# Optimization experiments

Measured on AMD Instinct MI355X. Metric: run time of the kernel, lower is better.

The kernel has to match this reference:

```python
import jax, jax.numpy as jnp
import numpy as np

C_, A_, B_ = 1, 128, 128          # image_size
H, Z, T, N = 512, 128, 16, 32     # h_dim, z_dim, steps, attention grid
EPS = 1e-8
BATCH = 256
PATCH = C_ * N * N                # read/write patch size (C_=1)
IN_ENC = 2 * PATCH + H


def gru_cell(x, h, W_ih, W_hh, b_ih, b_hh):
    gi = x @ W_ih.T + b_ih
    gh = h @ W_hh.T + b_hh
    i_r, i_z, i_n = jnp.split(gi, 3, axis=-1)
    h_r, h_z, h_n = jnp.split(gh, 3, axis=-1)
    r = jax.nn.sigmoid(i_r + h_r)
    z = jax.nn.sigmoid(i_z + h_z)
    n = jnp.tanh(i_n + r * h_n)
    return (1.0 - z) * n + z * h


def filterbank(gt, delta, two_sigma_sq, num_pixels):
    # gt, delta: [b,1]; two_sigma_sq: [b,1,1]
    g = 0.5 * (num_pixels + 1) * (gt + 1.0)                       # [b,1]
    grid = jnp.arange(N, dtype=jnp.float32) - 0.5 * (N - 1)       # [N]
    mu = g + grid[None, :] * delta                                # [b,N]
    pix = jnp.arange(num_pixels, dtype=jnp.float32)               # [P]
    F = jnp.exp(-(pix[None, None, :] - mu[:, :, None]) ** 2 / two_sigma_sq)
    return F / jnp.maximum(F.sum(axis=-1, keepdims=True), EPS)    # [b,N,P]


def get_filterbanks(h_dec, W_attn, b_attn):
    p = h_dec @ W_attn.T + b_attn                                 # [b,5]
    gt_x, gt_y, log_ss, log_dt, log_g = [p[:, i:i + 1] for i in range(5)]
    two_sigma_sq = (2.0 * jnp.exp(log_ss))[:, :, None]            # [b,1,1]
    delta = (max(A_, B_) - 1) * jnp.exp(log_dt) / (N - 1)         # [b,1]
    gamma = jnp.exp(log_g)                                        # [b,1]
    F_x = filterbank(gt_x, delta, two_sigma_sq, A_)               # [b,N,A]
    F_y = filterbank(gt_y, delta, two_sigma_sq, B_)               # [b,N,B]
    return F_x, F_y, gamma


def draw_forward(x, eps, W_ih_enc, W_hh_enc, b_ih_enc, b_hh_enc,
                 W_ih_dec, W_hh_dec, b_ih_dec, b_hh_dec,
                 W_mu, b_mu, W_ls, b_ls, W_wr, b_wr,
                 W_ra, b_ra, W_wa, b_wa):
    b = x.shape[0]
    xf = x.reshape(b, -1)                                         # [b, A*B]
    reconsts0 = jnp.zeros_like(xf)
    h0 = jnp.zeros((b, H), dtype=xf.dtype)

    def step(carry, eps_t):
        reconsts, h_enc, h_dec = carry
        # NOTE: faithful to original: reconsts[-1] is last batch row, broadcast
        x_hat = xf - jax.nn.sigmoid(reconsts[-1])
        # ---- read with attention ----
        F_x, F_y, gamma = get_filterbanks(h_dec, W_ra, b_ra)
        F_x_t = jnp.swapaxes(F_x, -1, -2)                         # [b,A,N]
        img = xf.reshape(b, A_, B_)
        img_hat = x_hat.reshape(b, A_, B_)
        x_attn = (F_y @ img @ F_x_t).reshape(b, -1)               # [b,N*N]
        xh_attn = (F_y @ img_hat @ F_x_t).reshape(b, -1)
        r = gamma * jnp.concatenate([x_attn, xh_attn], axis=1)    # [b,2*N*N]
        # ---- encoder GRU ----
        h_enc = gru_cell(jnp.concatenate([r, h_dec], axis=1), h_enc,
                         W_ih_enc, W_hh_enc, b_ih_enc, b_hh_enc)
        # ---- sample z ~ Q ----
        mu = h_enc @ W_mu.T + b_mu
        sigma = jnp.exp(h_enc @ W_ls.T + b_ls)
        z = mu + eps_t * sigma
        # ---- decoder GRU ----
        h_dec = gru_cell(z, h_dec, W_ih_dec, W_hh_dec, b_ih_dec, b_hh_dec)
        # ---- write with attention ----
        F_xw, F_yw, gamma_w = get_filterbanks(h_dec, W_wa, b_wa)
        w = (h_dec @ W_wr.T + b_wr).reshape(b, N, N)
        wr = (jnp.swapaxes(F_yw, -1, -2) @ w @ F_xw).reshape(b, -1) / gamma_w
        return (reconsts + wr, h_enc, h_dec), None

    (reconsts, _, _), _ = jax.lax.scan(step, (reconsts0, h0, h0), eps)
    return jax.nn.sigmoid(reconsts).reshape(-1, C_, A_, B_)


def setup_inputs() -> dict:
    key = jax.random.key(0)
    ks = jax.random.split(key, 24)
    s = 0.02
    inp = {
        "x": jax.random.uniform(ks[0], (BATCH, C_, A_, B_), jnp.float32),
        "eps": jax.random.normal(ks[1], (T, BATCH, Z), jnp.float32),
        "W_ih_enc": jax.random.normal(ks[2], (3 * H, IN_ENC), jnp.float32) * s,
        "W_hh_enc": jax.random.normal(ks[3], (3 * H, H), jnp.float32) * s,
        "b_ih_enc": jnp.zeros((3 * H,), jnp.float32),
        "b_hh_enc": jnp.zeros((3 * H,), jnp.float32),
        "W_ih_dec": jax.random.normal(ks[4], (3 * H, Z), jnp.float32) * s,
        "W_hh_dec": jax.random.normal(ks[5], (3 * H, H), jnp.float32) * s,
        "b_ih_dec": jnp.zeros((3 * H,), jnp.float32),
        "b_hh_dec": jnp.zeros((3 * H,), jnp.float32),
        "W_mu": jax.random.normal(ks[6], (Z, H), jnp.float32) * s,
        "b_mu": jnp.zeros((Z,), jnp.float32),
        "W_ls": jax.random.normal(ks[7], (Z, H), jnp.float32) * s,
        "b_ls": jnp.zeros((Z,), jnp.float32),
        "W_wr": jax.random.normal(ks[8], (PATCH, H), jnp.float32) * s,
        "b_wr": jnp.zeros((PATCH,), jnp.float32),
        "W_ra": jax.random.normal(ks[9], (5, H), jnp.float32) * s,
        "b_ra": jnp.zeros((5,), jnp.float32),
        "W_wa": jax.random.normal(ks[10], (5, H), jnp.float32) * s,
        "b_wa": jnp.zeros((5,), jnp.float32),
    }
    return inp


def reference(x, eps, W_ih_enc, W_hh_enc, b_ih_enc, b_hh_enc,
              W_ih_dec, W_hh_dec, b_ih_dec, b_hh_dec,
              W_mu, b_mu, W_ls, b_ls, W_wr, b_wr,
              W_ra, b_ra, W_wa, b_wa):
    return draw_forward(x, eps, W_ih_enc, W_hh_enc, b_ih_enc, b_hh_enc,
                        W_ih_dec, W_hh_dec, b_ih_dec, b_hh_dec,
                        W_mu, b_mu, W_ls, b_ls, W_wr, b_wr,
                        W_ra, b_ra, W_wa, b_wa)
```

## Files before the change

kernel.cpp:

```cpp
#include <hip/hip_runtime.h>
#include <math.h>

#define BATCHN 256
#define HDIM 512
#define ZDIM 128
#define NGRID 32
#define ABDIM 128
#define IMGSZ 16384
#define ENCIN 2560
#define G3 1536
#define SLAB (BATCHN*G3)

typedef __attribute__((ext_vector_type(8))) short short8;
typedef __attribute__((ext_vector_type(4))) float f32x4;

__device__ __forceinline__ float sigmoidf_(float x){ return 1.0f/(1.0f+expf(-x)); }

__device__ __forceinline__ ushort f2bf_rne(float f){
    union{float f; uint u;} x; x.f=f;
    uint r = (x.u + 0x7FFFu + ((x.u>>16)&1u)) >> 16;
    return (ushort)r;
}
__device__ __forceinline__ float bf2f(ushort h){
    union{uint u; float f;} y; y.u = ((uint)h)<<16;
    return y.f;
}

__global__ void init_slast_k(float* __restrict__ s_last){
    int i = blockIdx.x*256 + threadIdx.x;
    s_last[i] = 0.5f;
}

__global__ void conv_wh_k(const float* __restrict__ W, ushort* __restrict__ Wh, int n4){
    int i = blockIdx.x*256 + threadIdx.x;
    if(i>=n4) return;
    float4 v = ((const float4*)W)[i];
    ushort4 hv;
    hv.x=f2bf_rne(v.x); hv.y=f2bf_rne(v.y); hv.z=f2bf_rne(v.z); hv.w=f2bf_rne(v.w);
    ((ushort4*)Wh)[i] = hv;
}

__device__ __forceinline__ void stage_swz(const ushort* __restrict__ g, int K,
        int grow0, int kb, ushort* lds, int tid){
    int wv = tid>>6, lane = tid&63;
    #pragma unroll
    for(int q=0;q<2;q++){
        int instr = wv*2 + q;
        int rl = instr*8 + (lane>>3);
        int sc = (lane&7) ^ (lane>>3);
        const ushort* src = g + (size_t)(grow0+rl)*K + kb + sc*8;
        ushort* dst = lds + instr*512;
        __builtin_amdgcn_global_load_lds((const __attribute__((address_space(1))) void*)src,
                                         (__attribute__((address_space(3))) void*)dst, 16, 0, 0);
    }
}

__device__ __forceinline__ short8 lds_read_swz(const ushort* arr, int r, int slot){
    return *(const short8*)&arr[r*64 + ((slot ^ (r&7))<<3)];
}

__device__ __forceinline__ short8 lds_read_swz128(const ushort* arr, int r, int slot16){
    return lds_read_swz(arr + (slot16>>3)*4096, r, slot16&7);
}

__device__ __forceinline__ void attn_params_dev512(const float* __restrict__ h,
        const float* __restrict__ W, const float* __restrict__ bvec,
        float* red5, float* pp, int tid){
    float accp[5];
    #pragma unroll
    for(int i=0;i<5;i++) accp[i]=0.f;
    for(int k=tid;k<HDIM;k+=512){
        float hv = h[k];
        #pragma unroll
        for(int i=0;i<5;i++) accp[i] += hv*W[i*HDIM+k];
    }
    int wv = tid>>6;
    #pragma unroll
    for(int i=0;i<5;i++){
        float a = accp[i];
        #pragma unroll
        for(int o=32;o>0;o>>=1) a += __shfl_down(a,o);
        if((tid&63)==0) red5[i*8+wv]=a;
    }
    __syncthreads();
    if(tid<5){
        float s = bvec[tid];
        #pragma unroll
        for(int w2=0;w2<8;w2++) s += red5[tid*8+w2];
        pp[tid]=s;
    }
    __syncthreads();
}

__device__ __forceinline__ void fill_fb_T(float* fxT, float* fyT, const float* pp, int tid){
    float gx = 64.5f*(pp[0]+1.0f);
    float gy = 64.5f*(pp[1]+1.0f);
    float tss = 2.0f*expf(pp[2]);
    float delta = (127.0f/31.0f)*expf(pp[3]);
    int rr = tid>>3;
    int q  = tid&7;
    int j  = rr&31;
    bool isY = rr>=32;
    float mu = (isY?gy:gx) + ((float)j-15.5f)*delta;
    float v[16]; float s=0.f;
    #pragma unroll
    for(int i=0;i<16;i++){
        float d = (float)(q*16+i)-mu;
        float e = expf(-d*d/tss);
        v[i]=e; s+=e;
    }
    s += __shfl_xor(s,1); s += __shfl_xor(s,2); s += __shfl_xor(s,4);
    float inv = 1.0f/fmaxf(s,1e-8f);
    float* dst = isY? fyT : fxT;
    #pragma unroll
    for(int i=0;i<16;i++) dst[(q*16+i)*32 + j] = v[i]*inv;
    __syncthreads();
}

__device__ __forceinline__ void fill_fb_R(float (*fx)[ABDIM+1], float (*fy)[ABDIM+1], const float* pp, int tid){
    float gx = 64.5f*(pp[0]+1.0f);
    float gy = 64.5f*(pp[1]+1.0f);
    float tss = 2.0f*expf(pp[2]);
    float delta = (127.0f/31.0f)*expf(pp[3]);
    int rr = tid>>3;
    int q  = tid&7;
    int j  = rr&31;
    bool isY = rr>=32;
    float mu = (isY?gy:gx) + ((float)j-15.5f)*delta;
    float v[16]; float s=0.f;
    #pragma unroll
    for(int i=0;i<16;i++){
        float d = (float)(q*16+i)-mu;
        float e = expf(-d*d/tss);
        v[i]=e; s+=e;
    }
    s += __shfl_xor(s,1); s += __shfl_xor(s,2); s += __shfl_xor(s,4);
    float inv = 1.0f/fmaxf(s,1e-8f);
    float* rowp = isY? &fy[j][0] : &fx[j][0];
    #pragma unroll
    for(int i=0;i<16;i++) rowp[q*16+i] = v[i]*inv;
    __syncthreads();
}

__global__ __launch_bounds__(512) void read_attn_k(const float* __restrict__ xf, const float* __restrict__ s_last,
        const float* __restrict__ hdec, const ushort* __restrict__ Hd_h, const ushort* __restrict__ Hd_l,
        const float* __restrict__ W_ra, const float* __restrict__ b_ra,
        ushort* __restrict__ Eh, ushort* __restrict__ El){
    __shared__ float smem[4096 + 8256 + 48];
    float* sFxT = smem;
    float* sFyT = smem + 4096;
    float* tmp  = smem + 4096;
    float* red5 = smem + 4096 + 8256;
    float* pp   = red5 + 40;
    int bb = blockIdx.x >> 1, half = blockIdx.x & 1;
    int tid = threadIdx.x;
    const float* h = hdec + bb*HDIM;
    attn_params_dev512(h, W_ra, b_ra, red5, pp, tid);
    float gamma = expf(pp[4]);
    fill_fb_T(sFxT, sFyT, pp, tid);

    const float* img = xf + (size_t)bb*IMGSZ;
    int c = tid & 127;
    int jg = tid >> 7;
    int jbase = half*16 + jg*4;
    float acc0[4], accS[4];
    #pragma unroll
    for(int i=0;i<4;i++){ acc0[i]=0.f; accS[i]=0.f; }
    for(int k=0;k<ABDIM;k++){
        float s  = img[k*ABDIM + c];
        float sl = s_last[k*ABDIM + c];
        float4 f0 = *(const float4*)&sFyT[k*32 + jbase];
        acc0[0]+=f0.x*s;  acc0[1]+=f0.y*s;  acc0[2]+=f0.z*s;  acc0[3]+=f0.w*s;
        accS[0]+=f0.x*sl; accS[1]+=f0.y*sl; accS[2]+=f0.z*sl; accS[3]+=f0.w*sl;
    }
    __syncthreads();
    #pragma unroll
    for(int i=0;i<4;i++){
        int jl = jg*4+i;
        tmp[0*16*129 + jl*129 + c] = acc0[i];
        tmp[1*16*129 + jl*129 + c] = acc0[i] - accS[i];
    }
    __syncthreads();
    {
        int i2 = tid & 15;
        int jl = (tid>>4) & 15;
        int p  = tid >> 8;
        float a0=0.f, a1=0.f;
        for(int cc=0; cc<ABDIM; cc++){
            float tv = tmp[p*16*129 + jl*129 + cc];
            a0 += tv*sFxT[cc*32 + i2*2];
            a1 += tv*sFxT[cc*32 + i2*2 + 1];
        }
        float o0 = gamma*a0, o1 = gamma*a1;
        int j = half*16 + jl;
        ushort h0=f2bf_rne(o0), h1=f2bf_rne(o1);
        ushort2 oh; oh.x=h0; oh.y=h1;
        ushort2 ol; ol.x=f2bf_rne(o0-bf2f(h0)); ol.y=f2bf_rne(o1-bf2f(h1));
        size_t off = (size_t)bb*ENCIN + p*1024 + j*NGRID + i2*2;
        *(ushort2*)(Eh + off) = oh;
        *(ushort2*)(El + off) = ol;
    }
    if(half==0){
        int i = tid;
        Eh[(size_t)bb*ENCIN + 2048 + i] = Hd_h[(size_t)bb*HDIM + i];
        El[(size_t)bb*ENCIN + 2048 + i] = Hd_l[(size_t)bb*HDIM + i];
    }
}

__device__ void gemm_one(const ushort* __restrict__ Agh, const ushort* __restrict__ Agl,
        const ushort* __restrict__ Wh,
        int K, int k0, int kiters, int row0, int col0, int Nn, float* __restrict__ Out,
        ushort* AH, ushort* AL, ushort* BH, int tid){
    int lane = tid&63, w = tid>>6;
    int m0 = (w>>1)*32, n0 = (w&1)*32;
    int fr = lane&15, sl = lane>>4;
    f32x4 acc[2][2];
    #pragma unroll
    for(int i=0;i<2;i++)
        #pragma unroll
        for(int j=0;j<2;j++) acc[i][j]=(f32x4){0.f,0.f,0.f,0.f};
    for(int it=0; it<kiters; ++it){
        int kb = k0 + it*128;
        stage_swz(Agh, K, row0, kb,    AH,      tid);
        stage_swz(Agh, K, row0, kb+64, AH+4096, tid);
        stage_swz(Agl, K, row0, kb,    AL,      tid);
        stage_swz(Agl, K, row0, kb+64, AL+4096, tid);
        stage_swz(Wh,  K, col0, kb,    BH,      tid);
        stage_swz(Wh,  K, col0, kb+64, BH+4096, tid);
        __syncthreads();
        #pragma unroll
        for(int ks=0; ks<4; ks++){
            int slot = ks*4 + sl;
            short8 a_h[2], a_l[2], b_h[2];
            #pragma unroll
            for(int mf=0;mf<2;mf++){
                a_h[mf] = lds_read_swz128(AH, m0+mf*16+fr, slot);
                a_l[mf] = lds_read_swz128(AL, m0+mf*16+fr, slot);
            }
            #pragma unroll
            for(int nf=0;nf<2;nf++)
                b_h[nf] = lds_read_swz128(BH, n0+nf*16+fr, slot);
            #pragma unroll
            for(int mf=0;mf<2;mf++)
                #pragma unroll
                for(int nf=0;nf<2;nf++){
                    acc[mf][nf] = __builtin_amdgcn_mfma_f32_16x16x32_bf16(a_h[mf], b_h[nf], acc[mf][nf], 0,0,0);
                    acc[mf][nf] = __builtin_amdgcn_mfma_f32_16x16x32_bf16(a_l[mf], b_h[nf], acc[mf][nf], 0,0,0);
                }
        }
        __syncthreads();
    }
    int crow = (lane>>4)*4, ccol = lane&15;
    #pragma unroll
    for(int mf=0;mf<2;mf++)
        #pragma unroll
        for(int nf=0;nf<2;nf++)
            #pragma unroll
            for(int r=0;r<4;r++)
                Out[(size_t)(row0+m0+mf*16+crow+r)*Nn + col0+n0+nf*16+ccol] = acc[mf][nf][r];
}

__global__ __launch_bounds__(256) void gemm3_k(
        const ushort* __restrict__ Eh, const ushort* __restrict__ El,
        const ushort* __restrict__ Wie_h,
        const ushort* __restrict__ He_h, const ushort* __restrict__ He_l,
        const ushort* __restrict__ Whe_h,
        const ushort* __restrict__ Hd_h, const ushort* __restrict__ Hd_l,
        const ushort* __restrict__ Whd_h,
        float* __restrict__ Pi, float* __restrict__ Ph, float* __restrict__ Ph2){
    __shared__ ushort AH[2*64*64], AL[2*64*64], BH[2*64*64];
    int job = blockIdx.x, tid = threadIdx.x;
    if(job < 384){
        int tile = job % 96, s = job / 96;
        gemm_one(Eh, El, Wie_h, ENCIN, s*640, 5,
                 (tile/24)*64, (tile%24)*64, G3, Pi + (size_t)s*SLAB, AH, AL, BH, tid);
    } else if(job < 480){
        int tile = job - 384;
        gemm_one(He_h, He_l, Whe_h, HDIM, 0, 4,
                 (tile/24)*64, (tile%24)*64, G3, Ph, AH, AL, BH, tid);
    } else {
        int tile = job - 480;
        gemm_one(Hd_h, Hd_l, Whd_h, HDIM, 0, 4,
                 (tile/24)*64, (tile%24)*64, G3, Ph2, AH, AL, BH, tid);
    }
}

__global__ __launch_bounds__(256) void gemm_wr_k(
        const ushort* __restrict__ Hd_h, const ushort* __restrict__ Hd_l,
        const ushort* __restrict__ Wwr_h,
        float* __restrict__ Pw){
    __shared__ ushort AH[2*64*64], AL[2*64*64], BH[2*64*64];
    int tid = threadIdx.x;
    int r0 = blockIdx.y*64, c0 = blockIdx.x*64, s = blockIdx.z;
    gemm_one(Hd_h, Hd_l, Wwr_h, HDIM, s*256, 2, r0, c0, 1024,
             Pw + (size_t)s*BATCHN*1024, AH, AL, BH, tid);
}

__global__ __launch_bounds__(512) void combine_z_k(const float* __restrict__ Pi, const float* __restrict__ Ph,
        const float* __restrict__ bi, const float* __restrict__ bh,
        float* __restrict__ h, ushort* __restrict__ Hh, ushort* __restrict__ Hl,
        const float* __restrict__ Wmu, const float* __restrict__ bmu,
        const float* __restrict__ Wls, const float* __restrict__ bls,
        const float* __restrict__ eps_t, ushort* __restrict__ Zh, ushort* __restrict__ Zl){
    __shared__ float hs[HDIM];
    int bb = blockIdx.x, tid = threadIdx.x;
    int j = tid;
    float gi_r=bi[j], gi_z=bi[512+j], gi_n=bi[1024+j];
    float gh_r=bh[j], gh_z=bh[512+j], gh_n=bh[1024+j];
    #pragma unroll
    for(int s=0;s<4;s++){
        size_t base = (size_t)s*SLAB + (size_t)bb*G3 + j;
        gi_r += Pi[base]; gi_z += Pi[base+512]; gi_n += Pi[base+1024];
    }
    {
        size_t base = (size_t)bb*G3 + j;
        gh_r += Ph[base]; gh_z += Ph[base+512]; gh_n += Ph[base+1024];
    }
    float r = sigmoidf_(gi_r + gh_r);
    float z = sigmoidf_(gi_z + gh_z);
    float n = tanhf(gi_n + r*gh_n);
    size_t hoff = (size_t)bb*HDIM + j;
    float hn = (1.f - z)*n + z*h[hoff];
    h[hoff] = hn; hs[j] = hn;
    ushort hh = f2bf_rne(hn);
    Hh[hoff] = hh; Hl[hoff] = f2bf_rne(hn - bf2f(hh));
    __syncthreads();
    {
        int wv = tid>>6, lane = tid&63;
        const float4* hs4 = (const float4*)hs;
        float4 h0 = hs4[lane*2];
        float4 h1 = hs4[lane*2+1];
        #pragma unroll 4
        for(int it=0; it<16; ++it){
            int jo = wv*16 + it;
            const float4* wm = (const float4*)(Wmu + (size_t)jo*HDIM);
            const float4* wl = (const float4*)(Wls + (size_t)jo*HDIM);
            float4 m0=wm[lane*2], m1=wm[lane*2+1];
            float4 l0=wl[lane*2], l1=wl[lane*2+1];
            float am  = h0.x*m0.x+h0.y*m0.y+h0.z*m0.z+h0.w*m0.w
                      + h1.x*m1.x+h1.y*m1.y+h1.z*m1.z+h1.w*m1.w;
            float al_ = h0.x*l0.x+h0.y*l0.y+h0.z*l0.z+h0.w*l0.w
                      + h1.x*l1.x+h1.y*l1.y+h1.z*l1.z+h1.w*l1.w;
            #pragma unroll
            for(int o=32;o>0;o>>=1){ am += __shfl_down(am,o); al_ += __shfl_down(al_,o); }
            if(lane==0){
                float mu = am + bmu[jo];
                float sg = expf(al_ + bls[jo]);
                float zv = mu + eps_t[(size_t)bb*ZDIM + jo]*sg;
                ushort zh = f2bf_rne(zv);
                Zh[(size_t)bb*ZDIM + jo] = zh;
                Zl[(size_t)bb*ZDIM + jo] = f2bf_rne(zv - bf2f(zh));
            }
        }
    }
}

__global__ __launch_bounds__(256) void deci_combine_k(
        const ushort* __restrict__ Zh, const ushort* __restrict__ Zl,
        const ushort* __restrict__ Wid_h,
        const float* __restrict__ Ph2, const float* __restrict__ bi, const float* __restrict__ bh,
        float* __restrict__ h, ushort* __restrict__ Hh, ushort* __restrict__ Hl){
    __shared__ ushort AH[2*64*64], AL[2*64*64], BH[2*64*64];
    int tid = threadIdx.x;
    int lane = tid&63, w = tid>>6;
    int m0 = (w>>1)*32, n0 = (w&1)*32;
    int fr = lane&15, sl = lane>>4;
    int row0 = blockIdx.y*64;
    int jcol0 = blockIdx.x*64;
    f32x4 acc[3][2][2];
    #pragma unroll
    for(int g=0;g<3;g++)
        #pragma unroll
        for(int i=0;i<2;i++)
            #pragma unroll
            for(int jj=0;jj<2;jj++) acc[g][i][jj]=(f32x4){0.f,0.f,0.f,0.f};
    stage_swz(Zh, ZDIM, row0, 0,  AH,      tid);
    stage_swz(Zh, ZDIM, row0, 64, AH+4096, tid);
    stage_swz(Zl, ZDIM, row0, 0,  AL,      tid);
    stage_swz(Zl, ZDIM, row0, 64, AL+4096, tid);
    for(int g=0; g<3; ++g){
        if(g>0) __syncthreads();
        stage_swz(Wid_h, ZDIM, g*512 + jcol0, 0,  BH,      tid);
        stage_swz(Wid_h, ZDIM, g*512 + jcol0, 64, BH+4096, tid);
        __syncthreads();
        #pragma unroll
        for(int ks=0; ks<4; ks++){
            int slot = ks*4 + sl;
            short8 a_h[2], a_l[2], b_h[2];
            #pragma unroll
            for(int mf=0;mf<2;mf++){
                a_h[mf] = lds_read_swz128(AH, m0+mf*16+fr, slot);
                a_l[mf] = lds_read_swz128(AL, m0+mf*16+fr, slot);
            }
            #pragma unroll
            for(int nf=0;nf<2;nf++)
                b_h[nf] = lds_read_swz128(BH, n0+nf*16+fr, slot);
            #pragma unroll
            for(int mf=0;mf<2;mf++)
                #pragma unroll
                for(int nf=0;nf<2;nf++){
                    acc[g][mf][nf] = __builtin_amdgcn_mfma_f32_16x16x32_bf16(a_h[mf], b_h[nf], acc[g][mf][nf], 0,0,0);
                    acc[g][mf][nf] = __builtin_amdgcn_mfma_f32_16x16x32_bf16(a_l[mf], b_h[nf], acc[g][mf][nf], 0,0,0);
                }
        }
    }
    int crow = (lane>>4)*4, ccol = lane&15;
    #pragma unroll
    for(int mf=0;mf<2;mf++)
        #pragma unroll
        for(int nf=0;nf<2;nf++)
            #pragma unroll
            for(int r=0;r<4;r++){
                int row = row0 + m0 + mf*16 + crow + r;
                int col = jcol0 + n0 + nf*16 + ccol;
                size_t pbase = (size_t)row*G3 + col;
                float gi_r = acc[0][mf][nf][r] + bi[col];
                float gi_z = acc[1][mf][nf][r] + bi[512+col];
                float gi_n = acc[2][mf][nf][r] + bi[1024+col];
                float gh_r = Ph2[pbase]      + bh[col];
                float gh_z = Ph2[pbase+512]  + bh[512+col];
                float gh_n = Ph2[pbase+1024] + bh[1024+col];
                float rr = sigmoidf_(gi_r + gh_r);
                float zz = sigmoidf_(gi_z + gh_z);
                float nn = tanhf(gi_n + rr*gh_n);
                size_t idx = (size_t)row*HDIM + col;
                float hn = (1.f - zz)*nn + zz*h[idx];
                h[idx] = hn;
                ushort hh = f2bf_rne(hn);
                Hh[idx] = hh; Hl[idx] = f2bf_rne(hn - bf2f(hh));
            }
}

__global__ __launch_bounds__(512) void write_apply_k(const float* __restrict__ Pw, const float* __restrict__ b_wr,
        const float* __restrict__ hdec, const float* __restrict__ W_wa, const float* __restrict__ b_wa,
        float* __restrict__ rec, float* __restrict__ s_last, int last){
    __shared__ float sFy[NGRID][ABDIM+1];
    __shared__ float sFx[NGRID][ABDIM+1];
    __shared__ float sw[NGRID][36];
    __shared__ float t[64][36];
    __shared__ float red5[40];
    __shared__ float pp[8];
    int bb = blockIdx.x >> 1, half = blockIdx.x & 1;
    int p0 = half*64;
    int tid = threadIdx.x;
    const float* h = hdec + bb*HDIM;
    attn_params_dev512(h, W_wa, b_wa, red5, pp, tid);
    float invg = expf(-pp[4]);
    fill_fb_R(sFx, sFy, pp, tid);
    for(int i=tid;i<NGRID*NGRID;i+=512){
        float a = b_wr[i];
        #pragma unroll
        for(int s=0;s<2;s++) a += Pw[((size_t)s*BATCHN + bb)*1024 + i];
        sw[i>>5][i&31] = a;
    }
    __syncthreads();
    {
        int pl = tid>>3, iq = tid&7;
        int p = p0 + pl;
        float a[4];
        #pragma unroll
        for(int i=0;i<4;i++) a[i]=0.f;
        for(int j=0;j<NGRID;j++){
            float fy = sFy[j][p];
            float4 w0 = *(const float4*)&sw[j][iq*4];
            a[0]+=fy*w0.x; a[1]+=fy*w0.y; a[2]+=fy*w0.z; a[3]+=fy*w0.w;
        }
        float4 o0; o0.x=a[0];o0.y=a[1];o0.z=a[2];o0.w=a[3];
        *(float4*)&t[pl][iq*4] = o0;
    }
    __syncthreads();
    {
        int q = tid&127, pg = tid>>7;
        float fxc[32];
        #pragma unroll
        for(int i=0;i<32;i++) fxc[i] = sFx[i][q];
        for(int pi=0; pi<16; pi++){
            int pl = pg*16 + pi;
            int p = p0 + pl;
            float acc = 0.f;
            #pragma unroll
            for(int i4=0;i4<8;i4++){
                float4 tv = *(const float4*)&t[pl][i4*4];
                acc += tv.x*fxc[i4*4] + tv.y*fxc[i4*4+1] + tv.z*fxc[i4*4+2] + tv.w*fxc[i4*4+3];
            }
            size_t off = (size_t)bb*IMGSZ + p*ABDIM + q;
            float nv = rec[off] + acc*invg;
            rec[off] = last ? sigmoidf_(nv) : nv;
            if(bb==BATCHN-1) s_last[p*ABDIM + q] = sigmoidf_(nv);
        }
    }
}

extern "C" void kernel_launch(void* const* d_in, const int* in_sizes, int n_in,
                              void* d_out, int out_size, void* d_ws, size_t ws_size,
                              hipStream_t stream) {
    const float* x        = (const float*)d_in[0];
    const float* eps      = (const float*)d_in[1];
    const float* W_ih_enc = (const float*)d_in[2];
    const float* W_hh_enc = (const float*)d_in[3];
    const float* b_ih_enc = (const float*)d_in[4];
    const float* b_hh_enc = (const float*)d_in[5];
    const float* W_ih_dec = (const float*)d_in[6];
    const float* W_hh_dec = (const float*)d_in[7];
    const float* b_ih_dec = (const float*)d_in[8];
    const float* b_hh_dec = (const float*)d_in[9];
    const float* W_mu     = (const float*)d_in[10];
    const float* b_mu     = (const float*)d_in[11];
    const float* W_ls     = (const float*)d_in[12];
    const float* b_ls     = (const float*)d_in[13];
    const float* W_wr     = (const float*)d_in[14];
    const float* b_wr     = (const float*)d_in[15];
    const float* W_ra     = (const float*)d_in[16];
    const float* b_ra     = (const float*)d_in[17];
    const float* W_wa     = (const float*)d_in[18];
    const float* b_wa     = (const float*)d_in[19];

    float* rec = (float*)d_out;

    float* ws = (float*)d_ws;
    float* h_enc  = ws;  ws += BATCHN*HDIM;
    float* h_dec  = ws;  ws += BATCHN*HDIM;
    float* s_last = ws;  ws += IMGSZ;
    float* Pi     = ws;  ws += (size_t)4*SLAB;
    float* Ph     = ws;  ws += (size_t)SLAB;
    float* Ph2    = ws;  ws += (size_t)SLAB;
    float* Pw     = ws;  ws += (size_t)2*BATCHN*1024;

    ushort* us = (ushort*)ws;
    ushort* Wie_h = us; us += 1536*2560;
    ushort* Whe_h = us; us += 1536*512;
    ushort* Whd_h = us; us += 1536*512;
    ushort* Wid_h = us; us += 1536*128;
    ushort* Wwr_h = us; us += 1024*512;
    ushort* Eh    = us; us += BATCHN*ENCIN;
    ushort* El    = us; us += BATCHN*ENCIN;
    ushort* He_h  = us; us += BATCHN*HDIM;
    ushort* He_l  = us; us += BATCHN*HDIM;
    ushort* Hd_h  = us; us += BATCHN*HDIM;
    ushort* Hd_l  = us; us += BATCHN*HDIM;
    ushort* Zh    = us; us += BATCHN*ZDIM;
    ushort* Zl    = us; us += BATCHN*ZDIM;

    hipMemsetAsync(rec,   0, (size_t)BATCHN*IMGSZ*sizeof(float), stream);
    hipMemsetAsync(h_enc, 0, (size_t)BATCHN*HDIM*sizeof(float), stream);
    hipMemsetAsync(h_dec, 0, (size_t)BATCHN*HDIM*sizeof(float), stream);
    hipMemsetAsync(He_h,  0, (size_t)BATCHN*HDIM*sizeof(ushort)*2, stream);
    hipMemsetAsync(Hd_h,  0, (size_t)BATCHN*HDIM*sizeof(ushort)*2, stream);
    init_slast_k<<<IMGSZ/256,256,0,stream>>>(s_last);

    conv_wh_k<<<(1536*2560/4+255)/256,256,0,stream>>>(W_ih_enc, Wie_h, 1536*2560/4);
    conv_wh_k<<<(1536*512/4+255)/256,256,0,stream>>>(W_hh_enc, Whe_h, 1536*512/4);
    conv_wh_k<<<(1536*512/4+255)/256,256,0,stream>>>(W_hh_dec, Whd_h, 1536*512/4);
    conv_wh_k<<<(1536*128/4+255)/256,256,0,stream>>>(W_ih_dec, Wid_h, 1536*128/4);
    conv_wh_k<<<(1024*512/4+255)/256,256,0,stream>>>(W_wr, Wwr_h, 1024*512/4);

    for(int t=0;t<16;t++){
        read_attn_k<<<2*BATCHN,512,0,stream>>>(x, s_last, h_dec, Hd_h, Hd_l, W_ra, b_ra, Eh, El);
        gemm3_k<<<576,256,0,stream>>>(Eh, El, Wie_h, He_h, He_l, Whe_h,
                                      Hd_h, Hd_l, Whd_h, Pi, Ph, Ph2);
        combine_z_k<<<BATCHN,512,0,stream>>>(Pi, Ph, b_ih_enc, b_hh_enc,
            h_enc, He_h, He_l, W_mu, b_mu, W_ls, b_ls, eps + (size_t)t*BATCHN*ZDIM, Zh, Zl);
        deci_combine_k<<<dim3(8,4),256,0,stream>>>(Zh, Zl, Wid_h, Ph2,
            b_ih_dec, b_hh_dec, h_dec, Hd_h, Hd_l);
        gemm_wr_k<<<dim3(16,4,2),256,0,stream>>>(Hd_h, Hd_l, Wwr_h, Pw);
        write_apply_k<<<2*BATCHN,512,0,stream>>>(Pw, b_wr, h_dec, W_wa, b_wa, rec, s_last,
                                                 (t==15)?1:0);
    }
}
```

Baseline: 1.361 ms.

## Fuse decoder input GEMM and GRU update into the encoder combine kernel

Merges the separate MFMA-based decoder-input GEMM kernel into the per-batch-row encoder combine kernel. z stays in shared memory and each thread computes three gate dot products over 128 z values against a transposed bf16 W_ih_dec, then applies the decoder GRU update. This removes one launch per step and the Zh/Zl round trip through global memory. The cost is that the decoder input projection moves from MFMA to scalar FMAs, and each of 256 blocks re-reads the whole 128x1536 weight, though that should mostly hit cache.

```diff
diff --git a/kernel.cpp b/kernel.cpp
--- a/kernel.cpp
+++ b/kernel.cpp
@@ -38,6 +38,13 @@
     ushort4 hv;
     hv.x=f2bf_rne(v.x); hv.y=f2bf_rne(v.y); hv.z=f2bf_rne(v.z); hv.w=f2bf_rne(v.w);
     ((ushort4*)Wh)[i] = hv;
+}
+
+__global__ void conv_widT_k(const float* __restrict__ W, ushort* __restrict__ WT){
+    int i = blockIdx.x*256 + threadIdx.x;
+    if(i >= 128*1536) return;
+    int k = i / 1536, n = i % 1536;
+    WT[i] = f2bf_rne(W[n*128 + k]);
 }
 
 __device__ __forceinline__ void stage_swz(const ushort* __restrict__ g, int K,
@@ -296,34 +303,40 @@
              Pw + (size_t)s*BATCHN*1024, AH, AL, BH, tid);
 }
 
-__global__ __launch_bounds__(512) void combine_z_k(const float* __restrict__ Pi, const float* __restrict__ Ph,
-        const float* __restrict__ bi, const float* __restrict__ bh,
-        float* __restrict__ h, ushort* __restrict__ Hh, ushort* __restrict__ Hl,
+__global__ __launch_bounds__(512) void combine_all_k(const float* __restrict__ Pi, const float* __restrict__ Ph,
+        const float* __restrict__ bie, const float* __restrict__ bhe,
+        float* __restrict__ h_enc, ushort* __restrict__ Heh, ushort* __restrict__ Hel,
         const float* __restrict__ Wmu, const float* __restrict__ bmu,
         const float* __restrict__ Wls, const float* __restrict__ bls,
-        const float* __restrict__ eps_t, ushort* __restrict__ Zh, ushort* __restrict__ Zl){
+        const float* __restrict__ eps_t,
+        const ushort* __restrict__ WidT, const float* __restrict__ Ph2,
+        const float* __restrict__ bid_, const float* __restrict__ bhd,
+        float* __restrict__ h_dec, ushort* __restrict__ Hdh, ushort* __restrict__ Hdl){
     __shared__ float hs[HDIM];
+    __shared__ float zs[ZDIM];
     int bb = blockIdx.x, tid = threadIdx.x;
-    int j = tid;
-    float gi_r=bi[j], gi_z=bi[512+j], gi_n=bi[1024+j];
-    float gh_r=bh[j], gh_z=bh[512+j], gh_n=bh[1024+j];
-    #pragma unroll
-    for(int s=0;s<4;s++){
-        size_t base = (size_t)s*SLAB + (size_t)bb*G3 + j;
-        gi_r += Pi[base]; gi_z += Pi[base+512]; gi_n += Pi[base+1024];
-    }
     {
-        size_t base = (size_t)bb*G3 + j;
-        gh_r += Ph[base]; gh_z += Ph[base+512]; gh_n += Ph[base+1024];
-    }
-    float r = sigmoidf_(gi_r + gh_r);
-    float z = sigmoidf_(gi_z + gh_z);
-    float n = tanhf(gi_n + r*gh_n);
-    size_t hoff = (size_t)bb*HDIM + j;
-    float hn = (1.f - z)*n + z*h[hoff];
-    h[hoff] = hn; hs[j] = hn;
-    ushort hh = f2bf_rne(hn);
-    Hh[hoff] = hh; Hl[hoff] = f2bf_rne(hn - bf2f(hh));
+        int j = tid;
+        float gi_r=bie[j], gi_z=bie[512+j], gi_n=bie[1024+j];
+        float gh_r=bhe[j], gh_z=bhe[512+j], gh_n=bhe[1024+j];
+        #pragma unroll
+        for(int s=0;s<4;s++){
+            size_t base = (size_t)s*SLAB + (size_t)bb*G3 + j;
+            gi_r += Pi[base]; gi_z += Pi[base+512]; gi_n += Pi[base+1024];
+        }
+        {
+            size_t base = (size_t)bb*G3 + j;
+            gh_r += Ph[base]; gh_z += Ph[base+512]; gh_n += Ph[base+1024];
+        }
+        float r = sigmoidf_(gi_r + gh_r);
+        float z = sigmoidf_(gi_z + gh_z);
+        float n = tanhf(gi_n + r*gh_n);
+        size_t hoff = (size_t)bb*HDIM + j;
+        float hn = (1.f - z)*n + z*h_enc[hoff];
+        h_enc[hoff] = hn; hs[j] = hn;
+        ushort hh = f2bf_rne(hn);
+        Heh[hoff] = hh; Hel[hoff] = f2bf_rne(hn - bf2f(hh));
+    }
     __syncthreads();
     {
         int wv = tid>>6, lane = tid&63;
@@ -346,89 +359,38 @@
             if(lane==0){
                 float mu = am + bmu[jo];
                 float sg = expf(al_ + bls[jo]);
-                float zv = mu + eps_t[(size_t)bb*ZDIM + jo]*sg;
-                ushort zh = f2bf_rne(zv);
-                Zh[(size_t)bb*ZDIM + jo] = zh;
-                Zl[(size_t)bb*ZDIM + jo] = f2bf_rne(zv - bf2f(zh));
+                zs[jo] = mu + eps_t[(size_t)bb*ZDIM + jo]*sg;
             }
         }
     }
-}
-
-__global__ __launch_bounds__(256) void deci_combine_k(
-        const ushort* __restrict__ Zh, const ushort* __restrict__ Zl,
-        const ushort* __restrict__ Wid_h,
-        const float* __restrict__ Ph2, const float* __restrict__ bi, const float* __restrict__ bh,
-        float* __restrict__ h, ushort* __restrict__ Hh, ushort* __restrict__ Hl){
-    __shared__ ushort AH[2*64*64], AL[2*64*64], BH[2*64*64];
-    int tid = threadIdx.x;
-    int lane = tid&63, w = tid>>6;
-    int m0 = (w>>1)*32, n0 = (w&1)*32;
-    int fr = lane&15, sl = lane>>4;
-    int row0 = blockIdx.y*64;
-    int jcol0 = blockIdx.x*64;
-    f32x4 acc[3][2][2];
-    #pragma unroll
-    for(int g=0;g<3;g++)
-        #pragma unroll
-        for(int i=0;i<2;i++)
-            #pragma unroll
-            for(int jj=0;jj<2;jj++) acc[g][i][jj]=(f32x4){0.f,0.f,0.f,0.f};
-    stage_swz(Zh, ZDIM, row0, 0,  AH,      tid);
-    stage_swz(Zh, ZDIM, row0, 64, AH+4096, tid);
-    stage_swz(Zl, ZDIM, row0, 0,  AL,      tid);
-    stage_swz(Zl, ZDIM, row0, 64, AL+4096, tid);
-    for(int g=0; g<3; ++g){
-        if(g>0) __syncthreads();
-        stage_swz(Wid_h, ZDIM, g*512 + jcol0, 0,  BH,      tid);
-        stage_swz(Wid_h, ZDIM, g*512 + jcol0, 64, BH+4096, tid);
-        __syncthreads();
-        #pragma unroll
-        for(int ks=0; ks<4; ks++){
-            int slot = ks*4 + sl;
-            short8 a_h[2], a_l[2], b_h[2];
-            #pragma unroll
-            for(int mf=0;mf<2;mf++){
-                a_h[mf] = lds_read_swz128(AH, m0+mf*16+fr, slot);
-                a_l[mf] = lds_read_swz128(AL, m0+mf*16+fr, slot);
-            }
-            #pragma unroll
-            for(int nf=0;nf<2;nf++)
-                b_h[nf] = lds_read_swz128(BH, n0+nf*16+fr, slot);
-            #pragma unroll
-            for(int mf=0;mf<2;mf++)
-                #pragma unroll
-                for(int nf=0;nf<2;nf++){
-                    acc[g][mf][nf] = __builtin_amdgcn_mfma_f32_16x16x32_bf16(a_h[mf], b_h[nf], acc[g][mf][nf], 0,0,0);
-                    acc[g][mf][nf] = __builtin_amdgcn_mfma_f32_16x16x32_bf16(a_l[mf], b_h[nf], acc[g][mf][nf], 0,0,0);
-                }
-        }
-    }
-    int crow = (lane>>4)*4, ccol = lane&15;
-    #pragma unroll
-    for(int mf=0;mf<2;mf++)
-        #pragma unroll
-        for(int nf=0;nf<2;nf++)
-            #pragma unroll
-            for(int r=0;r<4;r++){
-                int row = row0 + m0 + mf*16 + crow + r;
-                int col = jcol0 + n0 + nf*16 + ccol;
-                size_t pbase = (size_t)row*G3 + col;
-                float gi_r = acc[0][mf][nf][r] + bi[col];
-                float gi_z = acc[1][mf][nf][r] + bi[512+col];
-                float gi_n = acc[2][mf][nf][r] + bi[1024+col];
-                float gh_r = Ph2[pbase]      + bh[col];
-                float gh_z = Ph2[pbase+512]  + bh[512+col];
-                float gh_n = Ph2[pbase+1024] + bh[1024+col];
-                float rr = sigmoidf_(gi_r + gh_r);
-                float zz = sigmoidf_(gi_z + gh_z);
-                float nn = tanhf(gi_n + rr*gh_n);
-                size_t idx = (size_t)row*HDIM + col;
-                float hn = (1.f - zz)*nn + zz*h[idx];
-                h[idx] = hn;
-                ushort hh = f2bf_rne(hn);
-                Hh[idx] = hh; Hl[idx] = f2bf_rne(hn - bf2f(hh));
-            }
+    __syncthreads();
+    {
+        int nn = tid;
+        float gr=0.f, gz=0.f, gn=0.f;
+        #pragma unroll 4
+        for(int k=0;k<ZDIM;k++){
+            float zk = zs[k];
+            const ushort* wrow = WidT + (size_t)k*G3;
+            gr += zk*bf2f(wrow[nn]);
+            gz += zk*bf2f(wrow[512+nn]);
+            gn += zk*bf2f(wrow[1024+nn]);
+        }
+        size_t base = (size_t)bb*G3 + nn;
+        float gi_r = gr + bid_[nn];
+        float gi_z = gz + bid_[512+nn];
+        float gi_n = gn + bid_[1024+nn];
+        float gh_r = Ph2[base]      + bhd[nn];
+        float gh_z = Ph2[base+512]  + bhd[512+nn];
+        float gh_n = Ph2[base+1024] + bhd[1024+nn];
+        float rr = sigmoidf_(gi_r + gh_r);
+        float zz = sigmoidf_(gi_z + gh_z);
+        float nv = tanhf(gi_n + rr*gh_n);
+        size_t idx = (size_t)bb*HDIM + nn;
+        float hn = (1.f - zz)*nv + zz*h_dec[idx];
+        h_dec[idx] = hn;
+        ushort hh = f2bf_rne(hn);
+        Hdh[idx] = hh; Hdl[idx] = f2bf_rne(hn - bf2f(hh));
+    }
 }
 
 __global__ __launch_bounds__(512) void write_apply_k(const float* __restrict__ Pw, const float* __restrict__ b_wr,
@@ -530,7 +492,7 @@
     ushort* Wie_h = us; us += 1536*2560;
     ushort* Whe_h = us; us += 1536*512;
     ushort* Whd_h = us; us += 1536*512;
-    ushort* Wid_h = us; us += 1536*128;
+    ushort* WidT  = us; us += 128*1536;
     ushort* Wwr_h = us; us += 1024*512;
     ushort* Eh    = us; us += BATCHN*ENCIN;
     ushort* El    = us; us += BATCHN*ENCIN;
@@ -538,8 +500,6 @@
     ushort* He_l  = us; us += BATCHN*HDIM;
     ushort* Hd_h  = us; us += BATCHN*HDIM;
     ushort* Hd_l  = us; us += BATCHN*HDIM;
-    ushort* Zh    = us; us += BATCHN*ZDIM;
-    ushort* Zl    = us; us += BATCHN*ZDIM;
 
     hipMemsetAsync(rec,   0, (size_t)BATCHN*IMGSZ*sizeof(float), stream);
     hipMemsetAsync(h_enc, 0, (size_t)BATCHN*HDIM*sizeof(float), stream);
@@ -551,17 +511,16 @@
     conv_wh_k<<<(1536*2560/4+255)/256,256,0,stream>>>(W_ih_enc, Wie_h, 1536*2560/4);
     conv_wh_k<<<(1536*512/4+255)/256,256,0,stream>>>(W_hh_enc, Whe_h, 1536*512/4);
     conv_wh_k<<<(1536*512/4+255)/256,256,0,stream>>>(W_hh_dec, Whd_h, 1536*512/4);
-    conv_wh_k<<<(1536*128/4+255)/256,256,0,stream>>>(W_ih_dec, Wid_h, 1536*128/4);
+    conv_widT_k<<<(128*1536+255)/256,256,0,stream>>>(W_ih_dec, WidT);
     conv_wh_k<<<(1024*512/4+255)/256,256,0,stream>>>(W_wr, Wwr_h, 1024*512/4);
 
     for(int t=0;t<16;t++){
         read_attn_k<<<2*BATCHN,512,0,stream>>>(x, s_last, h_dec, Hd_h, Hd_l, W_ra, b_ra, Eh, El);
         gemm3_k<<<576,256,0,stream>>>(Eh, El, Wie_h, He_h, He_l, Whe_h,
                                       Hd_h, Hd_l, Whd_h, Pi, Ph, Ph2);
-        combine_z_k<<<BATCHN,512,0,stream>>>(Pi, Ph, b_ih_enc, b_hh_enc,
-            h_enc, He_h, He_l, W_mu, b_mu, W_ls, b_ls, eps + (size_t)t*BATCHN*ZDIM, Zh, Zl);
-        deci_combine_k<<<dim3(8,4),256,0,stream>>>(Zh, Zl, Wid_h, Ph2,
-            b_ih_dec, b_hh_dec, h_dec, Hd_h, Hd_l);
+        combine_all_k<<<BATCHN,512,0,stream>>>(Pi, Ph, b_ih_enc, b_hh_enc,
+            h_enc, He_h, He_l, W_mu, b_mu, W_ls, b_ls, eps + (size_t)t*BATCHN*ZDIM,
+            WidT, Ph2, b_ih_dec, b_hh_dec, h_dec, Hd_h, Hd_l);
         gemm_wr_k<<<dim3(16,4,2),256,0,stream>>>(Hd_h, Hd_l, Wwr_h, Pw);
         write_apply_k<<<2*BATCHN,512,0,stream>>>(Pw, b_wr, h_dec, W_wa, b_wa, rec, s_last,
                                                  (t==15)?1:0);
```

Result: slower. 1.397 ms (+2.7%).
